# Performance work log

Hardware: AMD Instinct MI355X
Metric: run time of the kernel (lower is better)

Reference implementation:

```python
import jax, jax.numpy as jnp
import numpy as np

TOP_K = 2  # cfg.MODEL.MOE.TOP_K


def setup_inputs() -> dict:
    key = jax.random.key(0)
    ks = jax.random.split(key, 5)
    bs, L, d_in, d_out, E = 32, 1024, 768, 256, 8
    return {
        "x": jax.random.normal(ks[0], (bs, L, d_in), dtype=jnp.float32),
        "gate_W": jax.random.normal(ks[1], (d_in, E), dtype=jnp.float32) * (1.0 / np.sqrt(d_in)),
        "gate_b": jax.random.normal(ks[2], (E,), dtype=jnp.float32) * 0.01,
        "expert_W": jax.random.normal(ks[3], (E, d_in, d_out), dtype=jnp.float32) * (1.0 / np.sqrt(d_in)),
        "expert_b": jax.random.normal(ks[4], (E, d_out), dtype=jnp.float32) * 0.01,
    }


def reference(x, gate_W, gate_b, expert_W, expert_b):
    # Gate: (bs, L, E) softmax over experts, then top-k routing weights.
    gate_logits = jnp.einsum("bli,ie->ble", x, gate_W) + gate_b
    gate_weights = jax.nn.softmax(gate_logits, axis=-1)
    topk_vals, topk_idx = jax.lax.top_k(gate_weights, TOP_K)  # (bs, L, K)

    # Dense all-expert projection (E is small), then gather the selected ones.
    # all_out: (bs, L, E, d_out)
    all_out = jnp.einsum("bli,eio->bleo", x, expert_W) + expert_b

    # Select top-k expert outputs per token: (bs, L, K, d_out)
    sel = jnp.take_along_axis(all_out, topk_idx[..., None], axis=2)

    # Weighted combine over the K routed experts -> (bs, L, d_out)
    output = jnp.sum(sel * topk_vals[..., None], axis=2)
    return output
```

## Files before the change

kernel.cpp:

```cpp
#include <hip/hip_runtime.h>
#include <hip/hip_bf16.h>
#include <stdint.h>

#define T_TOKENS 32768
#define D_IN     768
#define D_OUT    256
#define N_EXP    8
#define S_TOT    (T_TOKENS*2)
#define S_PAD    66560
#define KSPLIT   6
#define NKB      24

typedef __attribute__((ext_vector_type(8))) short bf16x8;
typedef __attribute__((ext_vector_type(4))) float f32x4;

__device__ __forceinline__ unsigned short f2bf(float f) {
    unsigned u = __float_as_uint(f);
    return (unsigned short)((u + 0x7FFFu + ((u >> 16) & 1u)) >> 16);
}
__device__ __forceinline__ unsigned pack_bf2(float a, float b) {
    return (unsigned)f2bf(a) | ((unsigned)f2bf(b) << 16);
}

__device__ __forceinline__ void async16(void* lds, const void* g) {
    __builtin_amdgcn_global_load_lds(
        (const __attribute__((address_space(1))) unsigned int*)g,
        (__attribute__((address_space(3))) unsigned int*)lds, 16, 0, 0);
}

__global__ __launch_bounds__(256) void convw_kernel(
        const float* __restrict__ W, unsigned short* __restrict__ WTb,
        int* __restrict__ zero16) {
    if (blockIdx.x == 0 && threadIdx.x < 16) zero16[threadIdx.x] = 0;
    int eb_ = blockIdx.x;
    int n = threadIdx.x;
    const float* src = W + ((size_t)(eb_ / NKB) * D_IN + (eb_ % NKB) * 32) * 256 + n;
    unsigned pk[16];
    #pragma unroll
    for (int j = 0; j < 16; j++)
        pk[j] = pack_bf2(src[(2*j) * 256], src[(2*j+1) * 256]);
    unsigned* dst = (unsigned*)(WTb + ((size_t)eb_ * 256 + n) * 32);
    #pragma unroll
    for (int j = 0; j < 16; j++) dst[j] = pk[j];
}

__global__ __launch_bounds__(64) void gate_partial_kernel(
        const float* __restrict__ x, const float* __restrict__ gW,
        unsigned short* __restrict__ xbf, float* __restrict__ partial) {
    __shared__ float tile[64 * 65];
    int tid = threadIdx.x;
    int t0  = blockIdx.x * 64;
    int kq  = blockIdx.y;
    int c16 = tid & 15, rb = tid >> 4;
    float acc[8] = {0,0,0,0,0,0,0,0};
    #pragma unroll 1
    for (int j = 0; j < 2; j++) {
        int kc = kq * 128 + j * 64;
        #pragma unroll
        for (int i = 0; i < 16; i++) {
            int row = i * 4 + rb;
            size_t g = (size_t)(t0 + row) * D_IN + kc + c16 * 4;
            float4 v = *(const float4*)(x + g);
            uint2 p; p.x = pack_bf2(v.x, v.y); p.y = pack_bf2(v.z, v.w);
            *(uint2*)(xbf + g) = p;
            float* d = &tile[row * 65 + c16 * 4];
            d[0] = v.x; d[1] = v.y; d[2] = v.z; d[3] = v.w;
        }
        __syncthreads();
        const float* gr = gW + (size_t)kc * 8;
        #pragma unroll 8
        for (int kk = 0; kk < 64; kk++) {
            float xv = tile[tid * 65 + kk];
            #pragma unroll
            for (int e = 0; e < 8; e++) acc[e] += xv * gr[kk * 8 + e];
        }
        __syncthreads();
    }
    float* dst = partial + ((size_t)kq * T_TOKENS + t0 + tid) * 8;
    float4 o0 = {acc[0], acc[1], acc[2], acc[3]};
    float4 o1 = {acc[4], acc[5], acc[6], acc[7]};
    *(float4*)dst = o0; *(float4*)(dst + 4) = o1;
}

__global__ __launch_bounds__(256) void gate_final_kernel(
        const float* __restrict__ partial, const float* __restrict__ gb,
        float* __restrict__ topk_w, int* __restrict__ topk_e, int* __restrict__ counts) {
    __shared__ int h[8];
    int tid = threadIdx.x;
    if (tid < 8) h[tid] = 0;
    __syncthreads();
    int t = blockIdx.x * 256 + tid;
    float acc[8] = {0,0,0,0,0,0,0,0};
    #pragma unroll
    for (int q = 0; q < KSPLIT; q++) {
        const float* p = partial + ((size_t)q * T_TOKENS + t) * 8;
        float4 a = *(const float4*)p;
        float4 b = *(const float4*)(p + 4);
        acc[0] += a.x; acc[1] += a.y; acc[2] += a.z; acc[3] += a.w;
        acc[4] += b.x; acc[5] += b.y; acc[6] += b.z; acc[7] += b.w;
    }
    float mx = -1e30f;
    #pragma unroll
    for (int e = 0; e < 8; e++) { acc[e] += gb[e]; mx = fmaxf(mx, acc[e]); }
    float w[8], s = 0.f;
    #pragma unroll
    for (int e = 0; e < 8; e++) { w[e] = expf(acc[e] - mx); s += w[e]; }
    float inv = 1.0f / s;
    int e0 = 0; float b0 = -1.f;
    #pragma unroll
    for (int e = 0; e < 8; e++) if (w[e] > b0) { b0 = w[e]; e0 = e; }
    int e1 = 0; float b1 = -1.f;
    #pragma unroll
    for (int e = 0; e < 8; e++) if (e != e0 && w[e] > b1) { b1 = w[e]; e1 = e; }
    topk_w[t*2]   = b0 * inv;
    topk_w[t*2+1] = b1 * inv;
    topk_e[t*2]   = e0;
    topk_e[t*2+1] = e1;
    atomicAdd(&h[e0], 1); atomicAdd(&h[e1], 1);
    __syncthreads();
    if (tid < 8) atomicAdd(&counts[tid], h[tid]);
}

__global__ void scatter_kernel(const int* __restrict__ topk_e, const float* __restrict__ topk_w,
                               const int* __restrict__ counts, int* __restrict__ cursors,
                               int* __restrict__ slot_token, float* __restrict__ slot_w) {
    int offs[9]; offs[0] = 0;
    #pragma unroll
    for (int e = 0; e < 8; e++) offs[e+1] = offs[e] + ((counts[e] + 127) & ~127);
    __shared__ int hcnt[8], hbase[8];
    if (threadIdx.x < 8) hcnt[threadIdx.x] = 0;
    __syncthreads();
    int idx[4], ee[4], lr[4];
    int base = blockIdx.x * 256 * 4 + threadIdx.x;
    #pragma unroll
    for (int j = 0; j < 4; j++) {
        idx[j] = base + j * 256;
        ee[j]  = topk_e[idx[j]];
        lr[j]  = atomicAdd(&hcnt[ee[j]], 1);
    }
    __syncthreads();
    if (threadIdx.x < 8) hbase[threadIdx.x] = atomicAdd(&cursors[threadIdx.x], hcnt[threadIdx.x]);
    __syncthreads();
    #pragma unroll
    for (int j = 0; j < 4; j++) {
        int slot = offs[ee[j]] + hbase[ee[j]] + lr[j];
        slot_token[slot] = idx[j] >> 1;
        slot_w[slot]     = topk_w[idx[j]];
    }
}

__global__ __launch_bounds__(256, 3) void moe_gemm_kernel(
        const unsigned short* __restrict__ xbf, const unsigned short* __restrict__ WTb,
        const float* __restrict__ eb, const int* __restrict__ counts,
        const int* __restrict__ slot_token, const float* __restrict__ slot_w,
        float* __restrict__ out) {
    __shared__ unsigned short A_lds[3][128 * 32];
    __shared__ unsigned short B_lds[3][128 * 32];

    int lbid = (blockIdx.x & 7) * ((int)gridDim.x >> 3) + (blockIdx.x >> 3);
    int ch   = lbid & 1;
    int trow = lbid >> 1;

    int offs[9]; offs[0] = 0;
    #pragma unroll
    for (int e = 0; e < 8; e++) offs[e+1] = offs[e] + ((counts[e] + 127) & ~127);
    int row0 = trow * 128;
    if (row0 >= offs[8]) return;
    int expert = 0;
    #pragma unroll
    for (int e = 0; e < 8; e++) if (row0 >= offs[e]) expert = e;

    int tid  = threadIdx.x;
    int wave = tid >> 6, lane = tid & 63;
    int lrow = lane & 15, lquad = lane >> 4;
    int wm = wave >> 1, wn = wave & 1;

    const unsigned short* asrc[2];
    #pragma unroll
    for (int i = 0; i < 2; i++) {
        int c = i * 256 + tid;
        int r = c >> 2, p = c & 3;
        int lc = (p - (r >> 1)) & 3;
        int tok = slot_token[row0 + r];
        tok = (tok < 0 || tok >= T_TOKENS) ? 0 : tok;
        asrc[i] = xbf + (size_t)tok * D_IN + lc * 8;
    }
    const unsigned short* bexp = WTb + (size_t)expert * NKB * 8192 + ch * 4096;
    int boff[2];
    #pragma unroll
    for (int i = 0; i < 2; i++) {
        int c = i * 256 + tid;
        int r = c >> 2, p = c & 3;
        int lc = (p - (r >> 1)) & 3;
        boff[i] = r * 32 + lc * 8;
    }

    int a_off[4], b_off[4];
    #pragma unroll
    for (int m = 0; m < 4; m++) {
        int r = wm * 64 + m * 16 + lrow;
        a_off[m] = r * 32 + ((lquad + (r >> 1)) & 3) * 8;
    }
    #pragma unroll
    for (int q = 0; q < 4; q++) {
        int r = wn * 64 + q * 16 + lrow;
        b_off[q] = r * 32 + ((lquad + (r >> 1)) & 3) * 8;
    }

    f32x4 acc[4][4];
    #pragma unroll
    for (int m = 0; m < 4; m++)
        #pragma unroll
        for (int q = 0; q < 4; q++) acc[m][q] = (f32x4){0,0,0,0};

    auto stage = [&](int kb, int st) {
        #pragma unroll
        for (int i = 0; i < 2; i++)
            async16(&A_lds[st][(i * 256 + tid) * 8], asrc[i] + kb * 32);
        const unsigned short* tb = bexp + (size_t)kb * 8192;
        #pragma unroll
        for (int i = 0; i < 2; i++)
            async16(&B_lds[st][(i * 256 + tid) * 8], tb + boff[i]);
    };

    stage(0, 0);
    stage(1, 1);
    for (int s = 0; s < NKB; s++) {
        if (s == NKB - 1) asm volatile("s_waitcnt vmcnt(0)" ::: "memory");
        else              asm volatile("s_waitcnt vmcnt(4)" ::: "memory");
        asm volatile("s_barrier" ::: "memory");
        if (s + 2 < NKB) stage(s + 2, (s + 2) % 3);
        int p = s % 3;
        bf16x8 a[4], b[4];
        #pragma unroll
        for (int m = 0; m < 4; m++) a[m] = *(const bf16x8*)&A_lds[p][a_off[m]];
        #pragma unroll
        for (int q = 0; q < 4; q++) b[q] = *(const bf16x8*)&B_lds[p][b_off[q]];
        __builtin_amdgcn_s_setprio(1);
        #pragma unroll
        for (int q = 0; q < 4; q++)
            #pragma unroll
            for (int m = 0; m < 4; m++)
                acc[m][q] = __builtin_amdgcn_mfma_f32_16x16x32_bf16(a[m], b[q], acc[m][q], 0, 0, 0);
        __builtin_amdgcn_s_setprio(0);
    }

    float bias_q[4];
    #pragma unroll
    for (int q = 0; q < 4; q++)
        bias_q[q] = eb[expert * D_OUT + ch * 128 + wn * 64 + q * 16 + lrow];
    #pragma unroll
    for (int m = 0; m < 4; m++) {
        #pragma unroll
        for (int r = 0; r < 4; r++) {
            int slot = row0 + wm * 64 + m * 16 + lquad * 4 + r;
            int tk   = slot_token[slot];
            float wgt = slot_w[slot];
            if (wgt != 0.f) {
                float* drow = out + (size_t)tk * D_OUT + ch * 128 + wn * 64;
                #pragma unroll
                for (int q = 0; q < 4; q++)
                    atomicAdd(drow + q * 16 + lrow, wgt * (acc[m][q][r] + bias_q[q]));
            }
        }
    }
}

extern "C" void kernel_launch(void* const* d_in, const int* in_sizes, int n_in,
                              void* d_out, int out_size, void* d_ws, size_t ws_size,
                              hipStream_t stream) {
    const float* x  = (const float*)d_in[0];
    const float* gW = (const float*)d_in[1];
    const float* gb = (const float*)d_in[2];
    const float* eW = (const float*)d_in[3];
    const float* eb = (const float*)d_in[4];
    float* out = (float*)d_out;
    char* ws = (char*)d_ws;

    float* topk_w      = (float*)(ws + 0);
    int*   topk_e      = (int*)  (ws + 262144);
    int*   counts      = (int*)  (ws + 524288);
    int*   cursors     = (int*)  (ws + 524320);
    int*   slot_token  = (int*)  (ws + 524416);
    float* slot_w      = (float*)(ws + 790656);
    float* partial     = (float*)(ws + 1319040);
    unsigned short* WTb= (unsigned short*)(ws + 7610496);
    unsigned short* xbf= (unsigned short*)(ws + 10756224);

    hipMemsetAsync(slot_token, 0, 532480, stream);
    hipMemsetAsync(out, 0, (size_t)out_size * sizeof(float), stream);

    convw_kernel       <<<N_EXP * NKB, 256, 0, stream>>>(eW, WTb, counts);
    gate_partial_kernel<<<dim3(T_TOKENS / 64, KSPLIT), 64, 0, stream>>>(x, gW, xbf, partial);
    gate_final_kernel  <<<T_TOKENS / 256, 256, 0, stream>>>(partial, gb, topk_w, topk_e, counts);
    scatter_kernel     <<<S_TOT / (256 * 4), 256, 0, stream>>>(topk_e, topk_w, counts, cursors,
                                                               slot_token, slot_w);
    moe_gemm_kernel<<<(S_PAD / 128) * 2, 256, 0, stream>>>(xbf, WTb, eb, counts,
                                                           slot_token, slot_w, out);
}
```

Measured before the change: 281.1 us.

## Widen MoE GEMM tile to full output width and drop slot memset

The grouped GEMM now uses 512-thread blocks computing a 128x256 tile covering all output columns, so each gathered A row is loaded once instead of twice across two column-half blocks. B staging LDS doubles, and the wait count is adjusted for the new number of async loads per stage. Separately, the 532KB memset of slot_token/slot_w is removed; scatter block 0 zeroes only the padding weights. Padding slot_token entries are left uninitialized, which is tolerated by the clamp and the zero-weight skip, but one block's padding zeroing is not ordered against other blocks. Fewer blocks with higher occupancy requirements may change latency hiding.

```diff
diff --git a/kernel.cpp b/kernel.cpp
--- a/kernel.cpp
+++ b/kernel.cpp
@@ -127,6 +127,13 @@
     int offs[9]; offs[0] = 0;
     #pragma unroll
     for (int e = 0; e < 8; e++) offs[e+1] = offs[e] + ((counts[e] + 127) & ~127);
+    if (blockIdx.x == 0) {
+        #pragma unroll
+        for (int e = 0; e < 8; e++) {
+            int start = offs[e] + counts[e];
+            for (int i = start + threadIdx.x; i < offs[e+1]; i += 256) slot_w[i] = 0.f;
+        }
+    }
     __shared__ int hcnt[8], hbase[8];
     if (threadIdx.x < 8) hcnt[threadIdx.x] = 0;
     __syncthreads();
@@ -149,22 +156,20 @@
     }
 }
 
-__global__ __launch_bounds__(256, 3) void moe_gemm_kernel(
+__global__ __launch_bounds__(512, 2) void moe_gemm_kernel(
         const unsigned short* __restrict__ xbf, const unsigned short* __restrict__ WTb,
         const float* __restrict__ eb, const int* __restrict__ counts,
         const int* __restrict__ slot_token, const float* __restrict__ slot_w,
         float* __restrict__ out) {
     __shared__ unsigned short A_lds[3][128 * 32];
-    __shared__ unsigned short B_lds[3][128 * 32];
+    __shared__ unsigned short B_lds[3][256 * 32];
 
     int lbid = (blockIdx.x & 7) * ((int)gridDim.x >> 3) + (blockIdx.x >> 3);
-    int ch   = lbid & 1;
-    int trow = lbid >> 1;
 
     int offs[9]; offs[0] = 0;
     #pragma unroll
     for (int e = 0; e < 8; e++) offs[e+1] = offs[e] + ((counts[e] + 127) & ~127);
-    int row0 = trow * 128;
+    int row0 = lbid * 128;
     if (row0 >= offs[8]) return;
     int expert = 0;
     #pragma unroll
@@ -173,23 +178,19 @@
     int tid  = threadIdx.x;
     int wave = tid >> 6, lane = tid & 63;
     int lrow = lane & 15, lquad = lane >> 4;
-    int wm = wave >> 1, wn = wave & 1;
-
-    const unsigned short* asrc[2];
+    int wm = wave >> 2, wn = wave & 3;
+
+    int ar = tid >> 2, ap = tid & 3;
+    int alc = (ap - (ar >> 1)) & 3;
+    int tok = slot_token[row0 + ar];
+    tok = (tok < 0 || tok >= T_TOKENS) ? 0 : tok;
+    const unsigned short* asrc = xbf + (size_t)tok * D_IN + alc * 8;
+
+    const unsigned short* bexp = WTb + (size_t)expert * NKB * 8192;
+    int boff[2];
     #pragma unroll
     for (int i = 0; i < 2; i++) {
-        int c = i * 256 + tid;
-        int r = c >> 2, p = c & 3;
-        int lc = (p - (r >> 1)) & 3;
-        int tok = slot_token[row0 + r];
-        tok = (tok < 0 || tok >= T_TOKENS) ? 0 : tok;
-        asrc[i] = xbf + (size_t)tok * D_IN + lc * 8;
-    }
-    const unsigned short* bexp = WTb + (size_t)expert * NKB * 8192 + ch * 4096;
-    int boff[2];
-    #pragma unroll
-    for (int i = 0; i < 2; i++) {
-        int c = i * 256 + tid;
+        int c = i * 512 + tid;
         int r = c >> 2, p = c & 3;
         int lc = (p - (r >> 1)) & 3;
         boff[i] = r * 32 + lc * 8;
@@ -214,20 +215,18 @@
         for (int q = 0; q < 4; q++) acc[m][q] = (f32x4){0,0,0,0};
 
     auto stage = [&](int kb, int st) {
+        async16(&A_lds[st][tid * 8], asrc + kb * 32);
+        const unsigned short* tb = bexp + (size_t)kb * 8192;
         #pragma unroll
         for (int i = 0; i < 2; i++)
-            async16(&A_lds[st][(i * 256 + tid) * 8], asrc[i] + kb * 32);
-        const unsigned short* tb = bexp + (size_t)kb * 8192;
-        #pragma unroll
-        for (int i = 0; i < 2; i++)
-            async16(&B_lds[st][(i * 256 + tid) * 8], tb + boff[i]);
+            async16(&B_lds[st][(i * 512 + tid) * 8], tb + boff[i]);
     };
 
     stage(0, 0);
     stage(1, 1);
     for (int s = 0; s < NKB; s++) {
         if (s == NKB - 1) asm volatile("s_waitcnt vmcnt(0)" ::: "memory");
-        else              asm volatile("s_waitcnt vmcnt(4)" ::: "memory");
+        else              asm volatile("s_waitcnt vmcnt(3)" ::: "memory");
         asm volatile("s_barrier" ::: "memory");
         if (s + 2 < NKB) stage(s + 2, (s + 2) % 3);
         int p = s % 3;
@@ -248,7 +247,7 @@
     float bias_q[4];
     #pragma unroll
     for (int q = 0; q < 4; q++)
-        bias_q[q] = eb[expert * D_OUT + ch * 128 + wn * 64 + q * 16 + lrow];
+        bias_q[q] = eb[expert * D_OUT + wn * 64 + q * 16 + lrow];
     #pragma unroll
     for (int m = 0; m < 4; m++) {
         #pragma unroll
@@ -257,7 +256,7 @@
             int tk   = slot_token[slot];
             float wgt = slot_w[slot];
             if (wgt != 0.f) {
-                float* drow = out + (size_t)tk * D_OUT + ch * 128 + wn * 64;
+                float* drow = out + (size_t)tk * D_OUT + wn * 64;
                 #pragma unroll
                 for (int q = 0; q < 4; q++)
                     atomicAdd(drow + q * 16 + lrow, wgt * (acc[m][q][r] + bias_q[q]));
@@ -287,7 +286,6 @@
     unsigned short* WTb= (unsigned short*)(ws + 7610496);
     unsigned short* xbf= (unsigned short*)(ws + 10756224);
 
-    hipMemsetAsync(slot_token, 0, 532480, stream);
     hipMemsetAsync(out, 0, (size_t)out_size * sizeof(float), stream);
 
     convw_kernel       <<<N_EXP * NKB, 256, 0, stream>>>(eW, WTb, counts);
@@ -295,6 +293,6 @@
     gate_final_kernel  <<<T_TOKENS / 256, 256, 0, stream>>>(partial, gb, topk_w, topk_e, counts);
     scatter_kernel     <<<S_TOT / (256 * 4), 256, 0, stream>>>(topk_e, topk_w, counts, cursors,
                                                                slot_token, slot_w);
-    moe_gemm_kernel<<<(S_PAD / 128) * 2, 256, 0, stream>>>(xbf, WTb, eb, counts,
-                                                           slot_token, slot_w, out);
-}
+    moe_gemm_kernel<<<S_PAD / 128, 512, 0, stream>>>(xbf, WTb, eb, counts,
+                                                     slot_token, slot_w, out);
+}
```

After: 293.8 us. +4.5%, slower.
